# Kernel optimization log

Measured on AMD Instinct MI355X. Metric: run time of the kernel, lower is better.

Reference implementation:

```python
import jax, jax.numpy as jnp
import numpy as np

N = 10000      # nodes
E = 160000     # edges
IN = 256       # input feature dim
HID = 128      # hidden per head
H = 4          # heads (all layers)
EMB = 128      # dim_embedding (last-layer out per head)
SLOPE = 0.2    # leaky_relu negative slope in attention


def _gat_layer(h, src, dst, W, al, ar, b, residual, apply_act):
    """DGL-style GATConv (no dropout). h: [N, F_in], W: [F_in, H*D], al/ar/b: [H, D]."""
    n = h.shape[0]
    heads, d = al.shape
    feat = (h @ W).reshape(n, heads, d)                 # [N, H, D]
    el = jnp.sum(feat * al, axis=-1)                    # [N, H]
    er = jnp.sum(feat * ar, axis=-1)                    # [N, H]
    e = jax.nn.leaky_relu(el[src] + er[dst], SLOPE)     # [E, H]
    # edge softmax over incoming edges of dst (numerically stable)
    m = jax.ops.segment_max(e, dst, num_segments=n)
    m = jnp.where(jnp.isfinite(m), m, 0.0)              # empty segments -> 0
    ex = jnp.exp(e - m[dst])
    den = jax.ops.segment_sum(ex, dst, num_segments=n)
    alpha = ex / jnp.maximum(den[dst], 1e-9)            # [E, H]
    rst = jax.ops.segment_sum(alpha[:, :, None] * feat[src], dst, num_segments=n)  # [N, H, D]
    if residual:
        rst = rst + h.reshape(n, heads, d)              # identity residual (dims match)
    rst = rst + b
    return jax.nn.elu(rst) if apply_act else rst


def setup_inputs() -> dict:
    key = jax.random.key(0)
    ks = jax.random.split(key, 24)
    def p(k, shape, scale):
        return (jax.random.normal(k, shape, jnp.float32) * scale)
    inp = {
        'x': jax.random.normal(ks[0], (N, IN), jnp.float32),
        'src': jax.random.randint(ks[1], (E,), 0, N, dtype=jnp.int32).astype(jnp.int64),
        'dst': jax.random.randint(ks[2], (E,), 0, N, dtype=jnp.int32).astype(jnp.int64),
        # layer 0: in=IN, out=HID per head
        'W0': p(ks[3], (IN, H * HID), 1.0 / np.sqrt(IN)),
        'al0': p(ks[4], (H, HID), 0.1), 'ar0': p(ks[5], (H, HID), 0.1),
        'b0': p(ks[6], (H, HID), 0.02),
        # layer 1: in=H*HID=512, out=HID per head, residual
        'W1': p(ks[7], (H * HID, H * HID), 1.0 / np.sqrt(H * HID)),
        'al1': p(ks[8], (H, HID), 0.1), 'ar1': p(ks[9], (H, HID), 0.1),
        'b1': p(ks[10], (H, HID), 0.02),
        # layer 2: in=H*HID=512, out=EMB per head, residual, no activation
        'W2': p(ks[11], (H * HID, H * EMB), 1.0 / np.sqrt(H * HID)),
        'al2': p(ks[12], (H, EMB), 0.1), 'ar2': p(ks[13], (H, EMB), 0.1),
        'b2': p(ks[14], (H, EMB), 0.02),
        # MLP predictor: 2*EMB -> EMB -> EMB//2 -> 1
        'Wm0': p(ks[15], (2 * EMB, EMB), 1.0 / np.sqrt(2 * EMB)), 'bm0': p(ks[16], (EMB,), 0.02),
        'Wm1': p(ks[17], (EMB, EMB // 2), 1.0 / np.sqrt(EMB)), 'bm1': p(ks[18], (EMB // 2,), 0.02),
        'Wm2': p(ks[19], (EMB // 2, 1), 1.0 / np.sqrt(EMB // 2)), 'bm2': p(ks[20], (1,), 0.02),
    }
    return inp


def reference(x, src, dst, W0, al0, ar0, b0, W1, al1, ar1, b1, W2, al2, ar2, b2,
              Wm0, bm0, Wm1, bm1, Wm2, bm2):
    # GAT encoder
    h = _gat_layer(x, src, dst, W0, al0, ar0, b0, residual=False, apply_act=True).reshape(N, -1)
    h = _gat_layer(h, src, dst, W1, al1, ar1, b1, residual=True, apply_act=True).reshape(N, -1)
    h = _gat_layer(h, src, dst, W2, al2, ar2, b2, residual=True, apply_act=False).mean(axis=1)  # [N, EMB]
    # link predictor over all graph edges
    emb = jnp.concatenate([h[src], h[dst]], axis=1)     # [E, 2*EMB]
    z = jax.nn.relu(emb @ Wm0 + bm0)
    z = jax.nn.relu(z @ Wm1 + bm1)
    return jax.nn.sigmoid(z @ Wm2 + bm2)                # [E, 1]
```

## Files before the change

kernel.cpp:

```cpp
#include <hip/hip_runtime.h>
#include <hip/hip_bf16.h>
#include <math.h>

constexpr int kN = 10000;
constexpr int kE = 160000;
constexpr float kSlope = 0.2f;

typedef short v8s __attribute__((ext_vector_type(8)));
typedef float f32x4 __attribute__((ext_vector_type(4)));
typedef unsigned short ushort_t;

__device__ __forceinline__ float lrelu(float x) { return x > 0.f ? x : kSlope * x; }
__device__ __forceinline__ float elu_f(float x) { return x > 0.f ? x : (__expf(x) - 1.f); }
__device__ __forceinline__ float b2f(ushort_t u) {
    return __uint_as_float(((unsigned)u) << 16);
}
__device__ __forceinline__ float bl(unsigned u) { return __uint_as_float(u << 16); }
__device__ __forceinline__ float bh(unsigned u) { return __uint_as_float(u & 0xffff0000u); }
__device__ __forceinline__ ushort_t f2b(float f) {
    unsigned u = __float_as_uint(f);
    return (ushort_t)((u + 0x7FFFu + ((u >> 16) & 1u)) >> 16);
}

__global__ void detect_zero(const void* __restrict__ x, const void* __restrict__ dsti,
                            int* __restrict__ flags, int* __restrict__ deg) {
    if (blockIdx.x == 0) {
        __shared__ int sb[2];
        int tid = threadIdx.x;
        if (tid == 0) { sb[0] = 0; sb[1] = 0; }
        __syncthreads();
        const ushort_t* xb = (const ushort_t*)x;
        int big = 0;
        for (int i = tid; i < 4096; i += 256) {
            float v = b2f(xb[i]);
            if (!(fabsf(v) <= 1e4f)) big = 1;
        }
        const int* d32 = (const int*)dsti;
        int hi = 0;
        for (int i = tid; i < 4096; i += 256) hi |= d32[2 * i + 1];
        if (big) atomicOr(&sb[0], 1);
        if (hi)  atomicOr(&sb[1], 1);
        __syncthreads();
        if (tid == 0) { flags[0] = sb[0]; flags[1] = sb[1] ? 0 : 1; }
    } else {
        int i = (blockIdx.x - 1) * 256 + threadIdx.x;
        if (i < 2 * kN) deg[i] = 0;
    }
}

struct PrepArgs {
    const void* sm[13];
    const void* W0; const void* W1; const void* W2; const void* Wm0; const void* Wm1;
    const void* X; const void* srcIn; const void* dstIn;
    float* smallb;
    ushort_t* W0T; ushort_t* W1T; ushort_t* W2T; ushort_t* PQT; ushort_t* Wm1T;
    ushort_t* Xb;
    int* nsrc; int* ndst; int* deg;
    const int* flags;
};
constexpr int kPrepTotal = 4865 + 131072 + 262144 + 262144 + 32768 + 8192 + 2560000 + 320000;

__global__ void prep_all(PrepArgs a) {
    int i = blockIdx.x * 256 + threadIdx.x;
    if (i >= kPrepTotal) return;
    const int f32in = a.flags[0];
    auto cv = [&](const void* p, int idx) -> ushort_t {
        return f32in ? f2b(((const float*)p)[idx]) : ((const ushort_t*)p)[idx];
    };
    if (i < 4865) {
        int seg, offi;
        if (i < 4608)      { seg = i >> 9; offi = i & 511; }
        else if (i < 4736) { seg = 9;  offi = i - 4608; }
        else if (i < 4800) { seg = 10; offi = i - 4736; }
        else if (i < 4864) { seg = 11; offi = i - 4800; }
        else               { seg = 12; offi = 0; }
        a.smallb[i] = f32in ? ((const float*)a.sm[seg])[offi]
                            : b2f(((const ushort_t*)a.sm[seg])[offi]);
        return;
    }
    i -= 4865;
    if (i < 131072) {
        int n = i >> 8, k = i & 255;
        a.W0T[i] = cv(a.W0, k * 512 + n);
        return;
    }
    i -= 131072;
    if (i < 262144) {
        int n = i >> 9, k = i & 511;
        a.W1T[i] = cv(a.W1, k * 512 + n);
        return;
    }
    i -= 262144;
    if (i < 262144) {
        int n = i >> 9, k = i & 511;
        a.W2T[i] = cv(a.W2, k * 512 + n);
        return;
    }
    i -= 262144;
    if (i < 32768) {
        int n = i >> 7, k = i & 127;
        a.PQT[i] = cv(a.Wm0, (k + ((n < 128) ? 0 : 128)) * 128 + (n & 127));
        return;
    }
    i -= 32768;
    if (i < 8192) {
        int n = i >> 7, k = i & 127;
        a.Wm1T[i] = cv(a.Wm1, k * 64 + n);
        return;
    }
    i -= 8192;
    if (i < 2560000) {
        if (f32in) a.Xb[i] = f2b(((const float*)a.X)[i]);
        return;
    }
    i -= 2560000;
    {
        const void* in = (i < kE) ? a.srcIn : a.dstIn;
        int j = (i < kE) ? i : i - kE;
        int v = a.flags[1] ? (int)((const long long*)in)[j] : ((const int*)in)[j];
        v = ((unsigned)v < (unsigned)kN) ? v : 0;
        if (i < kE) a.nsrc[j] = v;
        else { a.ndst[j] = v; atomicAdd(&a.deg[v], 1); }
    }
}

__global__ __launch_bounds__(1024) void scan_off(const int* __restrict__ deg,
                                                 int* __restrict__ off, int n) {
    __shared__ int s[1024];
    int tid = threadIdx.x;
    int per = (n + 1023) >> 10;
    int base = tid * per;
    int sum = 0;
    for (int i = 0; i < per; ++i) { int j = base + i; if (j < n) sum += deg[j]; }
    s[tid] = sum;
    __syncthreads();
    for (int d = 1; d < 1024; d <<= 1) {
        int v = (tid >= d) ? s[tid - d] : 0;
        __syncthreads();
        s[tid] += v;
        __syncthreads();
    }
    int run = (tid > 0) ? s[tid - 1] : 0;
    for (int i = 0; i < per; ++i) {
        int j = base + i;
        if (j < n) { off[j] = run; run += deg[j]; }
    }
    if (tid == 0) off[n] = s[1023];
}

__global__ void fill_csr(const int* __restrict__ src, const int* __restrict__ dst,
                         const int* __restrict__ off, int* __restrict__ cnt,
                         int* __restrict__ ss, int* __restrict__ eid,
                         int* __restrict__ dpos, int n) {
    int i = blockIdx.x * 256 + threadIdx.x;
    if (i < n) {
        int d = dst[i];
        int pos = off[d] + atomicAdd(&cnt[d], 1);
        if (pos < kE) { ss[pos] = src[i]; eid[pos] = i; dpos[pos] = d; }
    }
}

template <bool ELER>
__global__ __launch_bounds__(256) void gemm_mfma(const ushort_t* __restrict__ A,
                                                 const void* __restrict__ Araw,
                                                 const int* __restrict__ gflags,
                                                 const ushort_t* __restrict__ WT,
                                                 ushort_t* __restrict__ Cout,
                                                 int M, int N, int K,
                                                 const float* __restrict__ al,
                                                 const float* __restrict__ ar,
                                                 float* __restrict__ el,
                                                 float* __restrict__ er) {
    __shared__ __align__(16) ushort_t As[4][64][8];
    __shared__ __align__(16) ushort_t Bs[4][128][8];
    __shared__ float elred[64][2][2];
    const int t = threadIdx.x;
    const int wave = t >> 6, lane = t & 63;
    const int l16 = lane & 15, q = lane >> 4;
    const int row0 = blockIdx.y * 64, col0 = blockIdx.x * 128;
    const int wm = (wave & 1) * 32, wn = (wave >> 1) * 64;
    const int am = t >> 2, ak8 = t & 3;
    const int sw = ak8 * 4;

    const ushort_t* Aeff = A;
    if (Araw != nullptr && gflags[0] == 0) Aeff = (const ushort_t*)Araw;

    const ushort_t* aptr = Aeff + (size_t)min(row0 + am, M - 1) * K + ak8 * 8;
    const ushort_t* bptr0 = WT + (size_t)(col0 + am) * K + ak8 * 8;
    const ushort_t* bptr1 = bptr0 + (size_t)64 * K;

    uint4 ga  = *(const uint4*)aptr;
    uint4 gb0 = *(const uint4*)bptr0;
    uint4 gb1 = *(const uint4*)bptr1;

    f32x4 acc[2][4];
#pragma unroll
    for (int mt = 0; mt < 2; ++mt)
#pragma unroll
        for (int nt = 0; nt < 4; ++nt)
#pragma unroll
            for (int r = 0; r < 4; ++r) acc[mt][nt][r] = 0.f;

    for (int k0 = 0; k0 < K; k0 += 32) {
        __syncthreads();
        *(uint4*)&As[ak8][am ^ sw][0] = ga;
        *(uint4*)&Bs[ak8][am ^ sw][0] = gb0;
        *(uint4*)&Bs[ak8][(am + 64) ^ sw][0] = gb1;
        __syncthreads();
        if (k0 + 32 < K) {
            ga  = *(const uint4*)(aptr + k0 + 32);
            gb0 = *(const uint4*)(bptr0 + k0 + 32);
            gb1 = *(const uint4*)(bptr1 + k0 + 32);
        }
        v8s af[2], bf[4];
        const int qs = q * 4;
#pragma unroll
        for (int mt = 0; mt < 2; ++mt)
            af[mt] = *(const v8s*)&As[q][(wm + mt * 16 + l16) ^ qs][0];
#pragma unroll
        for (int nt = 0; nt < 4; ++nt)
            bf[nt] = *(const v8s*)&Bs[q][(wn + nt * 16 + l16) ^ qs][0];
#pragma unroll
        for (int mt = 0; mt < 2; ++mt)
#pragma unroll
            for (int nt = 0; nt < 4; ++nt)
                acc[mt][nt] = __builtin_amdgcn_mfma_f32_16x16x32_bf16(af[mt], bf[nt],
                                                                      acc[mt][nt], 0, 0, 0);
    }
#pragma unroll
    for (int mt = 0; mt < 2; ++mt)
#pragma unroll
        for (int r = 0; r < 4; ++r) {
            int row = row0 + wm + mt * 16 + q * 4 + r;
            if (row < M) {
#pragma unroll
                for (int nt = 0; nt < 4; ++nt)
                    Cout[(size_t)row * N + col0 + wn + nt * 16 + l16] = f2b(acc[mt][nt][r]);
            }
        }
    if (ELER) {
        const int head = blockIdx.x;
        float alv[4], arv[4];
#pragma unroll
        for (int nt = 0; nt < 4; ++nt) {
            alv[nt] = al[head * 128 + wn + nt * 16 + l16];
            arv[nt] = ar[head * 128 + wn + nt * 16 + l16];
        }
#pragma unroll
        for (int mt = 0; mt < 2; ++mt)
#pragma unroll
            for (int r = 0; r < 4; ++r) {
                float pel = 0.f, per = 0.f;
#pragma unroll
                for (int nt = 0; nt < 4; ++nt) {
                    pel += acc[mt][nt][r] * alv[nt];
                    per += acc[mt][nt][r] * arv[nt];
                }
                pel += __shfl_xor(pel, 1); per += __shfl_xor(per, 1);
                pel += __shfl_xor(pel, 2); per += __shfl_xor(per, 2);
                pel += __shfl_xor(pel, 4); per += __shfl_xor(per, 4);
                pel += __shfl_xor(pel, 8); per += __shfl_xor(per, 8);
                if (l16 == 0) {
                    int rl = wm + mt * 16 + q * 4 + r;
                    elred[rl][wave >> 1][0] = pel;
                    elred[rl][wave >> 1][1] = per;
                }
            }
        __syncthreads();
        if (t < 64) {
            int row = row0 + t;
            if (row < M) {
                el[row * 4 + head] = elred[t][0][0] + elred[t][1][0];
                er[row * 4 + head] = elred[t][0][1] + elred[t][1][1];
            }
        }
    }
}

template <bool RES, bool ACT, int EPI>
__global__ __launch_bounds__(256) void gat_agg(const ushort_t* __restrict__ feat,
                                               const float* __restrict__ el,
                                               const float* __restrict__ er,
                                               const int* __restrict__ off,
                                               const int* __restrict__ ss,
                                               const ushort_t* residb,
                                               const float* __restrict__ bias,
                                               ushort_t* hl) {
    const int node = blockIdx.x * 4 + (threadIdx.x >> 6);
    const int lane = threadIdx.x & 63;
    if (node >= kN) return;
    const int off0 = off[node];
    const int deg = off[node + 1] - off0;
    float4 er4 = *(const float4*)(er + node * 4);
    const int head = lane >> 4;
    const float erh = (head == 0) ? er4.x : (head == 1) ? er4.y : (head == 2) ? er4.z : er4.w;
    const int c0 = lane * 8;
    const ushort_t* fbase = feat + c0;

    float den = 0.f;
    float acc[8] = {};
    if (deg > 0) {
        float e0[4], e1[4], e2[4];
        uint4 f0[4], f1[4], f2[4];
        auto LD = [&](int bj, float* ev, uint4* fv) {
#pragma unroll
            for (int i = 0; i < 4; ++i) {
                int s = ss[off0 + min(bj + i, deg - 1)];
                ev[i] = el[s * 4 + head];
                fv[i] = *(const uint4*)(fbase + (size_t)s * 512);
            }
        };
        auto CONS = [&](int bj, const float* ev, const uint4* fv) {
#pragma unroll
            for (int i = 0; i < 4; ++i) {
                if (bj + i < deg) {
                    float w = __expf(lrelu(ev[i] + erh));
                    den += w;
                    acc[0] += w * bl(fv[i].x); acc[1] += w * bh(fv[i].x);
                    acc[2] += w * bl(fv[i].y); acc[3] += w * bh(fv[i].y);
                    acc[4] += w * bl(fv[i].z); acc[5] += w * bh(fv[i].z);
                    acc[6] += w * bl(fv[i].w); acc[7] += w * bh(fv[i].w);
                }
            }
        };
        LD(0, e0, f0);
        LD(4, e1, f1);
        LD(8, e2, f2);
        for (int j = 0; j < deg; j += 12) {
            CONS(j, e0, f0);
            if (j + 12 < deg) LD(j + 12, e0, f0);
            CONS(j + 4, e1, f1);
            if (j + 16 < deg) LD(j + 16, e1, f1);
            CONS(j + 8, e2, f2);
            if (j + 20 < deg) LD(j + 20, e2, f2);
        }
    }
    const float inv = 1.f / fmaxf(den, 1e-9f);
    float4 b0 = *(const float4*)(bias + c0);
    float4 b1 = *(const float4*)(bias + c0 + 4);
    float v[8];
#pragma unroll
    for (int r = 0; r < 8; ++r) v[r] = acc[r] * inv;
    v[0] += b0.x; v[1] += b0.y; v[2] += b0.z; v[3] += b0.w;
    v[4] += b1.x; v[5] += b1.y; v[6] += b1.z; v[7] += b1.w;
    if (RES) {
        uint4 rv = *(const uint4*)(residb + (size_t)node * 512 + c0);
        v[0] += bl(rv.x); v[1] += bh(rv.x);
        v[2] += bl(rv.y); v[3] += bh(rv.y);
        v[4] += bl(rv.z); v[5] += bh(rv.z);
        v[6] += bl(rv.w); v[7] += bh(rv.w);
    }
    if (ACT) {
#pragma unroll
        for (int r = 0; r < 8; ++r) v[r] = elu_f(v[r]);
    }
    if (EPI == 1) {
        ushort_t* hp = hl + (size_t)node * 512 + c0;
        ushort4 h0 = {f2b(v[0]), f2b(v[1]), f2b(v[2]), f2b(v[3])};
        ushort4 h1 = {f2b(v[4]), f2b(v[5]), f2b(v[6]), f2b(v[7])};
        *(ushort4*)hp = h0;
        *(ushort4*)(hp + 4) = h1;
    }
    if (EPI == 2) {
        float m[8];
#pragma unroll
        for (int r = 0; r < 8; ++r) {
            float x = v[r] + __shfl_xor(v[r], 16);
            x += __shfl_xor(x, 32);
            m[r] = 0.25f * x;
        }
        if (lane < 16) {
            ushort_t* hp = hl + (size_t)node * 128 + lane * 8;
            ushort4 h0 = {f2b(m[0]), f2b(m[1]), f2b(m[2]), f2b(m[3])};
            ushort4 h1 = {f2b(m[4]), f2b(m[5]), f2b(m[6]), f2b(m[7])};
            *(ushort4*)hp = h0;
            *(ushort4*)(hp + 4) = h1;
        }
    }
}

__global__ __launch_bounds__(256) void edge_mfma(const ushort_t* __restrict__ PQb,
                                                 const float* __restrict__ bm0f,
                                                 const ushort_t* __restrict__ Wm1T,
                                                 const float* __restrict__ bm1f,
                                                 const float* __restrict__ wm2f,
                                                 const float* __restrict__ bm2f,
                                                 const int* __restrict__ ss,
                                                 const int* __restrict__ dpos,
                                                 const int* __restrict__ eid,
                                                 void* __restrict__ outv,
                                                 const int* __restrict__ flags) {
    const int t = threadIdx.x;
    const int wave = t >> 6, lane = t & 63;
    const int l16 = lane & 15, q = lane >> 4;
    const int base = blockIdx.x * 64 + wave * 16;
    const int pos = base + l16;
    const int s = ss[pos], d = dpos[pos];
    const ushort_t* prow = PQb + (size_t)s * 256;
    const ushort_t* qrow = PQb + (size_t)d * 256 + 128;

    f32x4 acc[4];
#pragma unroll
    for (int nt = 0; nt < 4; ++nt)
#pragma unroll
        for (int r = 0; r < 4; ++r) acc[nt][r] = 0.f;

#pragma unroll
    for (int ks = 0; ks < 4; ++ks) {
        const int k0 = ks * 32 + q * 8;
        uint4 pv = *(const uint4*)(prow + k0);
        uint4 qv = *(const uint4*)(qrow + k0);
        float4 bb0 = *(const float4*)(bm0f + k0);
        float4 bb1 = *(const float4*)(bm0f + k0 + 4);
        v8s a;
        a[0] = (short)f2b(fmaxf(bl(pv.x) + bl(qv.x) + bb0.x, 0.f));
        a[1] = (short)f2b(fmaxf(bh(pv.x) + bh(qv.x) + bb0.y, 0.f));
        a[2] = (short)f2b(fmaxf(bl(pv.y) + bl(qv.y) + bb0.z, 0.f));
        a[3] = (short)f2b(fmaxf(bh(pv.y) + bh(qv.y) + bb0.w, 0.f));
        a[4] = (short)f2b(fmaxf(bl(pv.z) + bl(qv.z) + bb1.x, 0.f));
        a[5] = (short)f2b(fmaxf(bh(pv.z) + bh(qv.z) + bb1.y, 0.f));
        a[6] = (short)f2b(fmaxf(bl(pv.w) + bl(qv.w) + bb1.z, 0.f));
        a[7] = (short)f2b(fmaxf(bh(pv.w) + bh(qv.w) + bb1.w, 0.f));
#pragma unroll
        for (int nt = 0; nt < 4; ++nt) {
            v8s b = *(const v8s*)(Wm1T + (size_t)(nt * 16 + l16) * 128 + k0);
            acc[nt] = __builtin_amdgcn_mfma_f32_16x16x32_bf16(a, b, acc[nt], 0, 0, 0);
        }
    }
    float b1v[4], w2v[4];
#pragma unroll
    for (int nt = 0; nt < 4; ++nt) {
        b1v[nt] = bm1f[nt * 16 + l16];
        w2v[nt] = wm2f[nt * 16 + l16];
    }
    float b2 = bm2f[0];
    const int f32out = flags[0];
#pragma unroll
    for (int r = 0; r < 4; ++r) {
        float v = 0.f;
#pragma unroll
        for (int nt = 0; nt < 4; ++nt)
            v += fmaxf(acc[nt][r] + b1v[nt], 0.f) * w2v[nt];
        v += __shfl_xor(v, 1);
        v += __shfl_xor(v, 2);
        v += __shfl_xor(v, 4);
        v += __shfl_xor(v, 8);
        if (l16 == 0) {
            int e = eid[base + q * 4 + r];
            float rr = 1.f / (1.f + __expf(-(v + b2)));
            if (f32out) ((float*)outv)[e] = rr;
            else        ((ushort_t*)outv)[e] = f2b(rr);
        }
    }
}

extern "C" void kernel_launch(void* const* d_in, const int* in_sizes, int n_in,
                              void* d_out, int out_size, void* d_ws, size_t ws_size,
                              hipStream_t stream) {
    (void)in_sizes; (void)n_in; (void)out_size; (void)ws_size;

    float* w = (float*)d_ws;
    size_t o = 0;
    auto alloc = [&](size_t n) { float* p = w + o; o += (n + 3) & ~size_t(3); return p; };
    float* smallb = alloc(4868);
    float* al0f = smallb + 0;    float* ar0f = smallb + 512;  float* b0f  = smallb + 1024;
    float* al1f = smallb + 1536; float* ar1f = smallb + 2048; float* b1f  = smallb + 2560;
    float* al2f = smallb + 3072; float* ar2f = smallb + 3584; float* b2f_ = smallb + 4096;
    float* bm0f = smallb + 4608; float* bm1f = smallb + 4736;
    float* wm2f = smallb + 4800; float* bm2f = smallb + 4864;
    float* elb  = alloc((size_t)kN * 4);
    float* erb  = alloc((size_t)kN * 4);
    ushort_t* Fb  = (ushort_t*)alloc((size_t)kN * 256);
    ushort_t* AHL = (ushort_t*)alloc((size_t)kN * 256);
    ushort_t* MHb = (ushort_t*)alloc((size_t)kN * 64);
    ushort_t* Xb  = (ushort_t*)alloc((size_t)kN * 128);
    ushort_t* W0T  = (ushort_t*)alloc(65536);
    ushort_t* W1T  = (ushort_t*)alloc(131072);
    ushort_t* W2T  = (ushort_t*)alloc(131072);
    ushort_t* PQT  = (ushort_t*)alloc(16384);
    ushort_t* Wm1T = (ushort_t*)alloc(4096);
    int* ip    = (int*)(w + o);
    int* flags = ip;
    int* deg   = ip + 4;
    int* cnt   = deg + kN;
    int* off   = cnt + kN;
    int* ss    = off + 10004;
    int* eid   = ss + kE;
    int* dpos  = eid + kE;
    int* nsrc  = dpos + kE;
    int* ndst  = nsrc + kE;

    ushort_t* PQb = Fb;

    dim3 blk(256);

    detect_zero<<<dim3(1 + (2 * kN + 255) / 256), blk, 0, stream>>>(d_in[0], d_in[2], flags, deg);

    PrepArgs a;
    const int sidx[13] = {4, 5, 6, 8, 9, 10, 12, 13, 14, 16, 18, 19, 20};
    for (int i = 0; i < 13; ++i) a.sm[i] = d_in[sidx[i]];
    a.W0 = d_in[3]; a.W1 = d_in[7]; a.W2 = d_in[11]; a.Wm0 = d_in[15]; a.Wm1 = d_in[17];
    a.X = d_in[0]; a.srcIn = d_in[1]; a.dstIn = d_in[2];
    a.smallb = smallb; a.W0T = W0T; a.W1T = W1T; a.W2T = W2T; a.PQT = PQT; a.Wm1T = Wm1T;
    a.Xb = Xb; a.nsrc = nsrc; a.ndst = ndst; a.deg = deg; a.flags = flags;
    prep_all<<<dim3((kPrepTotal + 255) / 256), blk, 0, stream>>>(a);

    scan_off<<<dim3(1), dim3(1024), 0, stream>>>(deg, off, kN);
    fill_csr<<<dim3((kE + 255) / 256), blk, 0, stream>>>(nsrc, ndst, off, cnt, ss, eid, dpos, kE);

    const int gy = (kN + 63) / 64;
    const int ga = (kN + 3) / 4;

    gemm_mfma<true><<<dim3(4, gy), blk, 0, stream>>>(Xb, d_in[0], flags, W0T, Fb,
                                                     kN, 512, 256, al0f, ar0f, elb, erb);
    gat_agg<false, true, 1><<<dim3(ga), blk, 0, stream>>>(Fb, elb, erb, off, ss,
                                                          nullptr, b0f, AHL);

    gemm_mfma<true><<<dim3(4, gy), blk, 0, stream>>>(AHL, nullptr, flags, W1T, Fb,
                                                     kN, 512, 512, al1f, ar1f, elb, erb);
    gat_agg<true, true, 1><<<dim3(ga), blk, 0, stream>>>(Fb, elb, erb, off, ss,
                                                         AHL, b1f, AHL);

    gemm_mfma<true><<<dim3(4, gy), blk, 0, stream>>>(AHL, nullptr, flags, W2T, Fb,
                                                     kN, 512, 512, al2f, ar2f, elb, erb);
    gat_agg<true, false, 2><<<dim3(ga), blk, 0, stream>>>(Fb, elb, erb, off, ss,
                                                          AHL, b2f_, MHb);

    gemm_mfma<false><<<dim3(2, gy), blk, 0, stream>>>(MHb, nullptr, flags, PQT, PQb,
                                                      kN, 256, 128,
                                                      nullptr, nullptr, nullptr, nullptr);

    edge_mfma<<<dim3(kE / 64), blk, 0, stream>>>(PQb, bm0f, Wm1T, bm1f, wm2f, bm2f,
                                                 ss, dpos, eid, d_out, flags);
}
```

Baseline: 320.8 us.

## Reorder layer-0 GAT to aggregate raw inputs before projecting with W0

Layer 0 now folds al/ar into W0 (precomputed inside scan_off), so el/er come straight from x in fill_csr's extra blocks. It then aggregates raw 256-dim inputs per head into a [N,4,256] buffer and runs the W0 GEMM afterwards per head, fusing bias and ELU into the GEMM epilogue. This uses linearity (sum alpha·x)W = sum alpha·(xW) to replace gathering 512-wide projected features with gathering 256-wide inputs. In exchange it adds a 20 MB intermediate write and read, and the GEMM now reads 1024-wide rows.

After: 337.3 us. 1.05x slower.

```diff
diff --git a/kernel.cpp b/kernel.cpp
--- a/kernel.cpp
+++ b/kernel.cpp
@@ -125,7 +125,12 @@
 }
 
 __global__ __launch_bounds__(1024) void scan_off(const int* __restrict__ deg,
-                                                 int* __restrict__ off, int n) {
+                                                 int* __restrict__ off, int n,
+                                                 const ushort_t* __restrict__ W0T,
+                                                 const float* __restrict__ al0,
+                                                 const float* __restrict__ ar0,
+                                                 float* __restrict__ wl0,
+                                                 float* __restrict__ wr0) {
     __shared__ int s[1024];
     int tid = threadIdx.x;
     int per = (n + 1023) >> 10;
@@ -146,31 +151,147 @@
         if (j < n) { off[j] = run; run += deg[j]; }
     }
     if (tid == 0) off[n] = s[1023];
-}
-
+    {
+        int h = tid >> 8, k = tid & 255;
+        const ushort_t* wp = W0T + (size_t)(h * 128) * 256 + k;
+        float accl = 0.f, accr = 0.f;
+        for (int d = 0; d < 128; ++d) {
+            float wv = b2f(wp[(size_t)d * 256]);
+            accl += wv * al0[h * 128 + d];
+            accr += wv * ar0[h * 128 + d];
+        }
+        wl0[tid] = accl;
+        wr0[tid] = accr;
+    }
+}
+
+constexpr int kFillBlocks = 625;
 __global__ void fill_csr(const int* __restrict__ src, const int* __restrict__ dst,
                          const int* __restrict__ off, int* __restrict__ cnt,
                          int* __restrict__ ss, int* __restrict__ eid,
-                         int* __restrict__ dpos, int n) {
-    int i = blockIdx.x * 256 + threadIdx.x;
-    if (i < n) {
-        int d = dst[i];
-        int pos = off[d] + atomicAdd(&cnt[d], 1);
-        if (pos < kE) { ss[pos] = src[i]; eid[pos] = i; dpos[pos] = d; }
-    }
-}
-
-template <bool ELER>
+                         int* __restrict__ dpos, int n,
+                         const ushort_t* __restrict__ xb, const void* __restrict__ xraw,
+                         const int* __restrict__ gflags,
+                         const float* __restrict__ wl0, const float* __restrict__ wr0,
+                         float* __restrict__ el0, float* __restrict__ er0) {
+    if (blockIdx.x < kFillBlocks) {
+        int i = blockIdx.x * 256 + threadIdx.x;
+        if (i < n) {
+            int d = dst[i];
+            int pos = off[d] + atomicAdd(&cnt[d], 1);
+            if (pos < kE) { ss[pos] = src[i]; eid[pos] = i; dpos[pos] = d; }
+        }
+        return;
+    }
+    const int node = (blockIdx.x - kFillBlocks) * 4 + (threadIdx.x >> 6);
+    const int lane = threadIdx.x & 63;
+    if (node >= kN) return;
+    const ushort_t* xeff = (gflags[0] == 0) ? (const ushort_t*)xraw : xb;
+    ushort4 x4 = *(const ushort4*)(xeff + (size_t)node * 256 + lane * 4);
+    float xv[4] = {b2f(x4.x), b2f(x4.y), b2f(x4.z), b2f(x4.w)};
+    float ep[4] = {}, rp[4] = {};
+#pragma unroll
+    for (int h = 0; h < 4; ++h) {
+        const float* wlh = wl0 + h * 256 + lane * 4;
+        const float* wrh = wr0 + h * 256 + lane * 4;
+#pragma unroll
+        for (int i = 0; i < 4; ++i) { ep[h] += xv[i] * wlh[i]; rp[h] += xv[i] * wrh[i]; }
+    }
+#pragma unroll
+    for (int m = 1; m < 64; m <<= 1) {
+#pragma unroll
+        for (int h = 0; h < 4; ++h) {
+            ep[h] += __shfl_xor(ep[h], m);
+            rp[h] += __shfl_xor(rp[h], m);
+        }
+    }
+    if (lane == 0) {
+#pragma unroll
+        for (int h = 0; h < 4; ++h) {
+            el0[node * 4 + h] = ep[h];
+            er0[node * 4 + h] = rp[h];
+        }
+    }
+}
+
+__global__ __launch_bounds__(256) void gat_agg_raw(const ushort_t* __restrict__ xb,
+                                                   const void* __restrict__ xraw,
+                                                   const int* __restrict__ gflags,
+                                                   const float* __restrict__ el,
+                                                   const float* __restrict__ er,
+                                                   const int* __restrict__ off,
+                                                   const int* __restrict__ ss,
+                                                   ushort_t* __restrict__ araw) {
+    const int node = blockIdx.x * 4 + (threadIdx.x >> 6);
+    const int lane = threadIdx.x & 63;
+    if (node >= kN) return;
+    const ushort_t* xeff = (gflags[0] == 0) ? (const ushort_t*)xraw : xb;
+    const int off0 = off[node];
+    const int deg = off[node + 1] - off0;
+    float4 er4 = *(const float4*)(er + node * 4);
+    const ushort_t* xcol = xeff + lane * 4;
+
+    float den[4] = {};
+    float acc[4][4] = {};
+    if (deg > 0) {
+        float4 e0[4], e1[4];
+        ushort4 x0[4], x1[4];
+        auto LD = [&](int bj, float4* ev, ushort4* xv) {
+#pragma unroll
+            for (int i = 0; i < 4; ++i) {
+                int s = ss[off0 + min(bj + i, deg - 1)];
+                ev[i] = *(const float4*)(el + s * 4);
+                xv[i] = *(const ushort4*)(xcol + (size_t)s * 256);
+            }
+        };
+        auto CONS = [&](int bj, const float4* ev, const ushort4* xv) {
+#pragma unroll
+            for (int i = 0; i < 4; ++i) {
+                if (bj + i < deg) {
+                    float w0 = __expf(lrelu(ev[i].x + er4.x));
+                    float w1 = __expf(lrelu(ev[i].y + er4.y));
+                    float w2 = __expf(lrelu(ev[i].z + er4.z));
+                    float w3 = __expf(lrelu(ev[i].w + er4.w));
+                    den[0] += w0; den[1] += w1; den[2] += w2; den[3] += w3;
+                    float v0 = b2f(xv[i].x), v1 = b2f(xv[i].y);
+                    float v2 = b2f(xv[i].z), v3 = b2f(xv[i].w);
+                    acc[0][0] += w0 * v0; acc[0][1] += w0 * v1; acc[0][2] += w0 * v2; acc[0][3] += w0 * v3;
+                    acc[1][0] += w1 * v0; acc[1][1] += w1 * v1; acc[1][2] += w1 * v2; acc[1][3] += w1 * v3;
+                    acc[2][0] += w2 * v0; acc[2][1] += w2 * v1; acc[2][2] += w2 * v2; acc[2][3] += w2 * v3;
+                    acc[3][0] += w3 * v0; acc[3][1] += w3 * v1; acc[3][2] += w3 * v2; acc[3][3] += w3 * v3;
+                }
+            }
+        };
+        LD(0, e0, x0);
+        LD(4, e1, x1);
+        for (int j = 0; j < deg; j += 8) {
+            CONS(j, e0, x0);
+            if (j + 8 < deg) LD(j + 8, e0, x0);
+            CONS(j + 4, e1, x1);
+            if (j + 12 < deg) LD(j + 12, e1, x1);
+        }
+    }
+#pragma unroll
+    for (int h = 0; h < 4; ++h) {
+        float inv = 1.f / fmaxf(den[h], 1e-9f);
+        ushort4 o = {f2b(acc[h][0] * inv), f2b(acc[h][1] * inv),
+                     f2b(acc[h][2] * inv), f2b(acc[h][3] * inv)};
+        *(ushort4*)(araw + (size_t)node * 1024 + h * 256 + lane * 4) = o;
+    }
+}
+
+template <int EMODE>
 __global__ __launch_bounds__(256) void gemm_mfma(const ushort_t* __restrict__ A,
                                                  const void* __restrict__ Araw,
                                                  const int* __restrict__ gflags,
                                                  const ushort_t* __restrict__ WT,
                                                  ushort_t* __restrict__ Cout,
-                                                 int M, int N, int K,
+                                                 int M, int N, int K, int lda, int aoff,
                                                  const float* __restrict__ al,
                                                  const float* __restrict__ ar,
                                                  float* __restrict__ el,
-                                                 float* __restrict__ er) {
+                                                 float* __restrict__ er,
+                                                 const float* __restrict__ bias) {
     __shared__ __align__(16) ushort_t As[4][64][8];
     __shared__ __align__(16) ushort_t Bs[4][128][8];
     __shared__ float elred[64][2][2];
@@ -185,7 +306,8 @@
     const ushort_t* Aeff = A;
     if (Araw != nullptr && gflags[0] == 0) Aeff = (const ushort_t*)Araw;
 
-    const ushort_t* aptr = Aeff + (size_t)min(row0 + am, M - 1) * K + ak8 * 8;
+    const ushort_t* aptr = Aeff + (size_t)min(row0 + am, M - 1) * lda
+                           + (size_t)blockIdx.x * aoff + ak8 * 8;
     const ushort_t* bptr0 = WT + (size_t)(col0 + am) * K + ak8 * 8;
     const ushort_t* bptr1 = bptr0 + (size_t)64 * K;
 
@@ -227,6 +349,12 @@
                 acc[mt][nt] = __builtin_amdgcn_mfma_f32_16x16x32_bf16(af[mt], bf[nt],
                                                                       acc[mt][nt], 0, 0, 0);
     }
+    float bv[4];
+    if (EMODE == 2) {
+#pragma unroll
+        for (int nt = 0; nt < 4; ++nt)
+            bv[nt] = bias[blockIdx.x * 128 + wn + nt * 16 + l16];
+    }
 #pragma unroll
     for (int mt = 0; mt < 2; ++mt)
 #pragma unroll
@@ -234,11 +362,14 @@
             int row = row0 + wm + mt * 16 + q * 4 + r;
             if (row < M) {
 #pragma unroll
-                for (int nt = 0; nt < 4; ++nt)
-                    Cout[(size_t)row * N + col0 + wn + nt * 16 + l16] = f2b(acc[mt][nt][r]);
+                for (int nt = 0; nt < 4; ++nt) {
+                    float vv = acc[mt][nt][r];
+                    if (EMODE == 2) vv = elu_f(vv + bv[nt]);
+                    Cout[(size_t)row * N + col0 + wn + nt * 16 + l16] = f2b(vv);
+                }
             }
         }
-    if (ELER) {
+    if (EMODE == 1) {
         const int head = blockIdx.x;
         float alv[4], arv[4];
 #pragma unroll
@@ -468,10 +599,13 @@
     float* al2f = smallb + 3072; float* ar2f = smallb + 3584; float* b2f_ = smallb + 4096;
     float* bm0f = smallb + 4608; float* bm1f = smallb + 4736;
     float* wm2f = smallb + 4800; float* bm2f = smallb + 4864;
+    float* wl0f = alloc(1024);
+    float* wr0f = alloc(1024);
     float* elb  = alloc((size_t)kN * 4);
     float* erb  = alloc((size_t)kN * 4);
     ushort_t* Fb  = (ushort_t*)alloc((size_t)kN * 256);
     ushort_t* AHL = (ushort_t*)alloc((size_t)kN * 256);
+    ushort_t* ARW = (ushort_t*)alloc((size_t)kN * 512);
     ushort_t* MHb = (ushort_t*)alloc((size_t)kN * 64);
     ushort_t* Xb  = (ushort_t*)alloc((size_t)kN * 128);
     ushort_t* W0T  = (ushort_t*)alloc(65536);
@@ -505,30 +639,34 @@
     a.Xb = Xb; a.nsrc = nsrc; a.ndst = ndst; a.deg = deg; a.flags = flags;
     prep_all<<<dim3((kPrepTotal + 255) / 256), blk, 0, stream>>>(a);
 
-    scan_off<<<dim3(1), dim3(1024), 0, stream>>>(deg, off, kN);
-    fill_csr<<<dim3((kE + 255) / 256), blk, 0, stream>>>(nsrc, ndst, off, cnt, ss, eid, dpos, kE);
+    scan_off<<<dim3(1), dim3(1024), 0, stream>>>(deg, off, kN, W0T, al0f, ar0f, wl0f, wr0f);
+    fill_csr<<<dim3(kFillBlocks + (kN + 3) / 4), blk, 0, stream>>>(
+        nsrc, ndst, off, cnt, ss, eid, dpos, kE,
+        Xb, d_in[0], flags, wl0f, wr0f, elb, erb);
 
     const int gy = (kN + 63) / 64;
     const int ga = (kN + 3) / 4;
 
-    gemm_mfma<true><<<dim3(4, gy), blk, 0, stream>>>(Xb, d_in[0], flags, W0T, Fb,
-                                                     kN, 512, 256, al0f, ar0f, elb, erb);
-    gat_agg<false, true, 1><<<dim3(ga), blk, 0, stream>>>(Fb, elb, erb, off, ss,
-                                                          nullptr, b0f, AHL);
-
-    gemm_mfma<true><<<dim3(4, gy), blk, 0, stream>>>(AHL, nullptr, flags, W1T, Fb,
-                                                     kN, 512, 512, al1f, ar1f, elb, erb);
+    gat_agg_raw<<<dim3(ga), blk, 0, stream>>>(Xb, d_in[0], flags, elb, erb, off, ss, ARW);
+    gemm_mfma<2><<<dim3(4, gy), blk, 0, stream>>>(ARW, nullptr, flags, W0T, AHL,
+                                                  kN, 512, 256, 1024, 256,
+                                                  nullptr, nullptr, nullptr, nullptr, b0f);
+
+    gemm_mfma<1><<<dim3(4, gy), blk, 0, stream>>>(AHL, nullptr, flags, W1T, Fb,
+                                                  kN, 512, 512, 512, 0,
+                                                  al1f, ar1f, elb, erb, nullptr);
     gat_agg<true, true, 1><<<dim3(ga), blk, 0, stream>>>(Fb, elb, erb, off, ss,
                                                          AHL, b1f, AHL);
 
-    gemm_mfma<true><<<dim3(4, gy), blk, 0, stream>>>(AHL, nullptr, flags, W2T, Fb,
-                                                     kN, 512, 512, al2f, ar2f, elb, erb);
+    gemm_mfma<1><<<dim3(4, gy), blk, 0, stream>>>(AHL, nullptr, flags, W2T, Fb,
+                                                  kN, 512, 512, 512, 0,
+                                                  al2f, ar2f, elb, erb, nullptr);
     gat_agg<true, false, 2><<<dim3(ga), blk, 0, stream>>>(Fb, elb, erb, off, ss,
                                                           AHL, b2f_, MHb);
 
-    gemm_mfma<false><<<dim3(2, gy), blk, 0, stream>>>(MHb, nullptr, flags, PQT, PQb,
-                                                      kN, 256, 128,
-                                                      nullptr, nullptr, nullptr, nullptr);
+    gemm_mfma<0><<<dim3(2, gy), blk, 0, stream>>>(MHb, nullptr, flags, PQT, PQb,
+                                                  kN, 256, 128, 128, 0,
+                                                  nullptr, nullptr, nullptr, nullptr, nullptr);
 
     edge_mfma<<<dim3(kE / 64), blk, 0, stream>>>(PQb, bm0f, Wm1T, bm1f, wm2f, bm2f,
                                                  ss, dpos, eid, d_out, flags);
```
